# Optimization experiments

Measured on AMD Instinct MI355X. Metric: run time of the kernel, lower is better.

## Reference

```python
import jax, jax.numpy as jnp
import numpy as np

N = 1024      # number of residues/tokens
D = 768       # node feature dim (heads * d_head)
H = 12        # heads
DH = D // H   # d_head = 64
DP = 128      # pair feature dim
SCALE = 0.125 # 1/sqrt(d_head)
EPS = 1e-5

def _ln(x, w, b):
    m = jnp.mean(x, axis=-1, keepdims=True)
    v = jnp.var(x, axis=-1, keepdims=True)
    return (x - m) * jax.lax.rsqrt(v + EPS) * w + b

def setup_inputs() -> dict:
    key = jax.random.key(0)
    ks = jax.random.split(key, 8)
    s = 0.02
    return {
        "node_feats": jax.random.normal(ks[0], (N, D), dtype=jnp.float32),
        "pair_feats": jax.random.normal(ks[1], (N, N, DP), dtype=jnp.float32),
        "ln_node_w": jnp.ones((D,), jnp.float32), "ln_node_b": jnp.zeros((D,), jnp.float32),
        "pair_ln_w": jnp.ones((DP,), jnp.float32), "pair_ln_b": jnp.zeros((DP,), jnp.float32),
        "qkv_W": jax.random.normal(ks[2], (D, 3 * D), dtype=jnp.float32) * s,
        "qkv_b": jnp.zeros((3 * D,), jnp.float32),
        "q_ln_w": jnp.ones((D,), jnp.float32), "q_ln_b": jnp.zeros((D,), jnp.float32),
        "k_ln_w": jnp.ones((D,), jnp.float32), "k_ln_b": jnp.zeros((D,), jnp.float32),
        "g_W": jax.random.normal(ks[3], (D, D), dtype=jnp.float32) * s,
        "g_b": jnp.zeros((D,), jnp.float32),
        "bias_W": jax.random.normal(ks[4], (DP, H), dtype=jnp.float32) * s,
        "bias_b": jnp.zeros((H,), jnp.float32),
        "out_W": jax.random.normal(ks[5], (D, D), dtype=jnp.float32) * s,
        "out_b": jnp.zeros((D,), jnp.float32),
        "mask": jax.random.bernoulli(ks[6], 0.9, (N, N)),
    }

def reference(node_feats, pair_feats, ln_node_w, ln_node_b, pair_ln_w, pair_ln_b,
              qkv_W, qkv_b, q_ln_w, q_ln_b, k_ln_w, k_ln_b,
              g_W, g_b, bias_W, bias_b, out_W, out_b, mask):
    x = _ln(node_feats, ln_node_w, ln_node_b)                 # [N, D]
    p = _ln(pair_feats, pair_ln_w, pair_ln_b)                 # [N, N, DP]
    q, k, v = jnp.split(x @ qkv_W + qkv_b, 3, axis=-1)        # each [N, D]
    q = _ln(q, q_ln_w, q_ln_b)
    k = _ln(k, k_ln_w, k_ln_b)
    g = x @ g_W + g_b                                         # [N, D]
    bias = jnp.einsum('ijp,ph->hij', p, bias_W) + bias_b[:, None, None]  # [H, N, N]
    bias = bias + jnp.where(mask[None, :, :], 0.0, -10000.0)
    q = q.reshape(N, H, DH); k = k.reshape(N, H, DH); v = v.reshape(N, H, DH)
    logits = jnp.einsum('ihd,jhd->hij', q, k) * SCALE + bias  # [H, N, N]
    attn = jax.nn.softmax(logits, axis=-1)
    out = jnp.einsum('hij,jhd->ihd', attn, v).reshape(N, D)   # [N, D]
    out = jax.nn.sigmoid(g) * out
    return out @ out_W + out_b
```

## Files before the change

### kernel.cpp

```cpp
#include <hip/hip_runtime.h>
#include <math.h>

#define N_TOK 1024
#define D_DIM 768
#define H_N   12
#define DH    64
#define DP    128
#define SCALE 0.125f
#define EPS   1e-5f
#define NN    (N_TOK * N_TOK)

__global__ __launch_bounds__(128) void prep_kernel(
    const float* __restrict__ pair_ln_w, const float* __restrict__ pair_ln_b,
    const float* __restrict__ bias_W, const float* __restrict__ bias_b,
    float* __restrict__ W2, float* __restrict__ S2cb)
{
    __shared__ float Ws[DP * H_N];
    __shared__ float slw[DP], slb[DP];
    int t = threadIdx.x;
    slw[t] = pair_ln_w[t];
    slb[t] = pair_ln_b[t];
    for (int idx = t; idx < DP * H_N; idx += 128) Ws[idx] = bias_W[idx];
    __syncthreads();
    for (int idx = t; idx < DP * H_N; idx += 128) {
        int c = idx / H_N;
        W2[idx] = slw[c] * Ws[idx];
    }
    if (t < 24) {
        int h = t % H_N;
        bool isS = t < H_N;
        float s = 0.f;
        for (int c = 0; c < DP; ++c)
            s += (isS ? slw[c] : slb[c]) * Ws[c * H_N + h];
        S2cb[t] = isS ? s : (s + bias_b[h]);
    }
}

__global__ __launch_bounds__(256) void ln_kernel(
    const float* __restrict__ in, float* __restrict__ out,
    int istride, int ostride,
    const float* __restrict__ w, const float* __restrict__ b)
{
    int row = blockIdx.x;
    int tid = threadIdx.x;
    const float* ip = in + (size_t)row * istride;
    float v0 = ip[tid], v1 = ip[tid + 256], v2 = ip[tid + 512];
    float s = v0 + v1 + v2;
    float q = v0 * v0 + v1 * v1 + v2 * v2;
    __shared__ float red[8];
    #pragma unroll
    for (int o = 32; o > 0; o >>= 1) {
        s += __shfl_down(s, o);
        q += __shfl_down(q, o);
    }
    int lane = tid & 63, wv = tid >> 6;
    if (lane == 0) { red[wv] = s; red[4 + wv] = q; }
    __syncthreads();
    if (tid == 0) {
        float ss = red[0] + red[1] + red[2] + red[3];
        float qq = red[4] + red[5] + red[6] + red[7];
        float mean = ss * (1.f / 768.f);
        float var = qq * (1.f / 768.f) - mean * mean;
        red[0] = mean;
        red[1] = rsqrtf(var + EPS);
    }
    __syncthreads();
    float mean = red[0], rstd = red[1];
    float* op = out + (size_t)row * ostride;
    op[tid]       = (v0 - mean) * rstd * w[tid]       + b[tid];
    op[tid + 256] = (v1 - mean) * rstd * w[tid + 256] + b[tid + 256];
    op[tid + 512] = (v2 - mean) * rstd * w[tid + 512] + b[tid + 512];
}

__global__ __launch_bounds__(256) void sgemm(
    const float* __restrict__ A, int lda,
    const float* __restrict__ B0, int ldb0, const float* __restrict__ bias0,
    const float* __restrict__ B1, int ldb1, const float* __restrict__ bias1,
    int split, float* __restrict__ C, int ldc, int K)
{
    __shared__ float As[16 * 68];
    __shared__ float Bs[16 * 68];
    int tid = threadIdx.x;
    int tx = tid & 15, ty = tid >> 4;
    int m0 = blockIdx.y * 64, n0 = blockIdx.x * 64;
    const float* Bp; const float* bp; int ldb, bcol0;
    if (n0 < split) { Bp = B0; bp = bias0; ldb = ldb0; bcol0 = n0; }
    else            { Bp = B1; bp = bias1; ldb = ldb1; bcol0 = n0 - split; }

    float acc[4][4] = {};
    int ar = tid >> 2, ak = (tid & 3) * 4;
    int bk = tid >> 4, bc = (tid & 15) * 4;

    for (int kt = 0; kt < K; kt += 16) {
        float4 av = *(const float4*)&A[(size_t)(m0 + ar) * lda + kt + ak];
        float4 bv = *(const float4*)&Bp[(size_t)(kt + bk) * ldb + bcol0 + bc];
        As[(ak + 0) * 68 + ar] = av.x;
        As[(ak + 1) * 68 + ar] = av.y;
        As[(ak + 2) * 68 + ar] = av.z;
        As[(ak + 3) * 68 + ar] = av.w;
        *(float4*)&Bs[bk * 68 + bc] = bv;
        __syncthreads();
        #pragma unroll
        for (int kk = 0; kk < 16; ++kk) {
            float4 a = *(const float4*)&As[kk * 68 + ty * 4];
            float4 b = *(const float4*)&Bs[kk * 68 + tx * 4];
            acc[0][0] += a.x * b.x; acc[0][1] += a.x * b.y; acc[0][2] += a.x * b.z; acc[0][3] += a.x * b.w;
            acc[1][0] += a.y * b.x; acc[1][1] += a.y * b.y; acc[1][2] += a.y * b.z; acc[1][3] += a.y * b.w;
            acc[2][0] += a.z * b.x; acc[2][1] += a.z * b.y; acc[2][2] += a.z * b.z; acc[2][3] += a.z * b.w;
            acc[3][0] += a.w * b.x; acc[3][1] += a.w * b.y; acc[3][2] += a.w * b.z; acc[3][3] += a.w * b.w;
        }
        __syncthreads();
    }
    float4 bb = *(const float4*)&bp[bcol0 + tx * 4];
    #pragma unroll
    for (int u = 0; u < 4; ++u) {
        float4 o;
        o.x = acc[u][0] + bb.x; o.y = acc[u][1] + bb.y;
        o.z = acc[u][2] + bb.z; o.w = acc[u][3] + bb.w;
        *(float4*)&C[(size_t)(m0 + ty * 4 + u) * ldc + n0 + tx * 4] = o;
    }
}

__global__ __launch_bounds__(256) void bias_kernel(
    const float* __restrict__ pair, const int* __restrict__ mask,
    const float* __restrict__ W2, const float* __restrict__ S2cb,
    float* __restrict__ biasbuf)
{
    __shared__ float sW2[DP * H_N];
    __shared__ float sS[H_N], sC[H_N];
    int tid = threadIdx.x;
    for (int t = tid; t < DP * H_N; t += 256) sW2[t] = W2[t];
    if (tid < H_N) { sS[tid] = S2cb[tid]; sC[tid] = S2cb[H_N + tid]; }
    __syncthreads();

    int gid = blockIdx.x * 256 + tid;
    const float4* p4 = (const float4*)(pair + (size_t)gid * DP);
    float sum = 0.f, ssq = 0.f;
    float dot[H_N];
    #pragma unroll
    for (int h = 0; h < H_N; ++h) dot[h] = 0.f;

    #pragma unroll 4
    for (int c4 = 0; c4 < 32; ++c4) {
        float4 v = p4[c4];
        float e[4] = { v.x, v.y, v.z, v.w };
        #pragma unroll
        for (int k = 0; k < 4; ++k) {
            float x = e[k];
            sum += x; ssq += x * x;
            const float* wp = &sW2[(c4 * 4 + k) * H_N];
            #pragma unroll
            for (int h = 0; h < H_N; ++h) dot[h] += x * wp[h];
        }
    }
    float mean = sum * (1.f / 128.f);
    float var  = ssq * (1.f / 128.f) - mean * mean;
    float rstd = rsqrtf(var + EPS);
    float mz = (mask[gid] != 0) ? 0.f : -10000.f;
    #pragma unroll
    for (int h = 0; h < H_N; ++h)
        biasbuf[(size_t)h * NN + gid] = (dot[h] - mean * sS[h]) * rstd + sC[h] + mz;
}

__global__ __launch_bounds__(256) void attn_kernel(
    const float* __restrict__ xw, const float* __restrict__ biasbuf,
    float* __restrict__ attn_out)
{
    const int h  = blockIdx.y;
    const int i0 = blockIdx.x * 16;
    const int tid = threadIdx.x;
    const int tx = tid & 15, ty = tid >> 4;

    __shared__ float Qs[16 * 65];
    __shared__ float Ks[32 * 65];
    __shared__ float Vs[32 * 68];
    __shared__ float Ps[16 * 33];

    {
        int r = tid >> 4, c4 = (tid & 15) * 4;
        float4 v = *(const float4*)(xw + (size_t)(i0 + r) * 3072 + h * 64 + c4);
        float* d = &Qs[r * 65 + c4];
        d[0] = v.x * SCALE; d[1] = v.y * SCALE; d[2] = v.z * SCALE; d[3] = v.w * SCALE;
    }

    float m = -1e30f, l = 0.f;
    float a0 = 0.f, a1 = 0.f, a2 = 0.f, a3 = 0.f;
    const float* brow = biasbuf + (size_t)h * NN + (size_t)(i0 + ty) * N_TOK;

    for (int j0 = 0; j0 < N_TOK; j0 += 32) {
        #pragma unroll
        for (int q2 = 0; q2 < 2; ++q2) {
            int idx = tid + q2 * 256;
            int r = idx >> 4, c4 = (idx & 15) * 4;
            const float* kb = xw + (size_t)(j0 + r) * 3072 + 768 + h * 64 + c4;
            float4 kv = *(const float4*)kb;
            float* kd = &Ks[r * 65 + c4];
            kd[0] = kv.x; kd[1] = kv.y; kd[2] = kv.z; kd[3] = kv.w;
            float4 vv = *(const float4*)(kb + 768);
            *(float4*)&Vs[r * 68 + c4] = vv;
        }
        __syncthreads();

        float s0 = 0.f, s1 = 0.f;
        const float* qrow = &Qs[ty * 65];
        const float* k0 = &Ks[(2 * tx) * 65];
        const float* k1 = k0 + 65;
        #pragma unroll
        for (int d = 0; d < 64; ++d) {
            float qv = qrow[d];
            s0 += qv * k0[d];
            s1 += qv * k1[d];
        }
        s0 += brow[j0 + 2 * tx];
        s1 += brow[j0 + 2 * tx + 1];

        float mt = fmaxf(s0, s1);
        #pragma unroll
        for (int o = 1; o < 16; o <<= 1) mt = fmaxf(mt, __shfl_xor(mt, o));
        float mn = fmaxf(m, mt);
        float al = __expf(m - mn);
        float p0 = __expf(s0 - mn);
        float p1 = __expf(s1 - mn);
        float rs = p0 + p1;
        #pragma unroll
        for (int o = 1; o < 16; o <<= 1) rs += __shfl_xor(rs, o);
        l = l * al + rs;
        m = mn;
        a0 *= al; a1 *= al; a2 *= al; a3 *= al;
        Ps[ty * 33 + 2 * tx]     = p0;
        Ps[ty * 33 + 2 * tx + 1] = p1;
        __syncthreads();

        const float* prow = &Ps[ty * 33];
        #pragma unroll
        for (int j = 0; j < 32; ++j) {
            float pv = prow[j];
            float4 vv = *(const float4*)&Vs[j * 68 + tx * 4];
            a0 += pv * vv.x; a1 += pv * vv.y; a2 += pv * vv.z; a3 += pv * vv.w;
        }
        __syncthreads();
    }

    float inv = 1.f / l;
    int row = i0 + ty;
    float4 gv = *(const float4*)(xw + (size_t)row * 3072 + 2304 + h * 64 + tx * 4);
    float* op = attn_out + (size_t)row * 768 + h * 64 + tx * 4;
    op[0] = a0 * inv / (1.f + __expf(-gv.x));
    op[1] = a1 * inv / (1.f + __expf(-gv.y));
    op[2] = a2 * inv / (1.f + __expf(-gv.z));
    op[3] = a3 * inv / (1.f + __expf(-gv.w));
}

extern "C" void kernel_launch(void* const* d_in, const int* in_sizes, int n_in,
                              void* d_out, int out_size, void* d_ws, size_t ws_size,
                              hipStream_t stream)
{
    const float* node      = (const float*)d_in[0];
    const float* pair      = (const float*)d_in[1];
    const float* ln_node_w = (const float*)d_in[2];
    const float* ln_node_b = (const float*)d_in[3];
    const float* pair_ln_w = (const float*)d_in[4];
    const float* pair_ln_b = (const float*)d_in[5];
    const float* qkv_W     = (const float*)d_in[6];
    const float* qkv_b     = (const float*)d_in[7];
    const float* q_ln_w    = (const float*)d_in[8];
    const float* q_ln_b    = (const float*)d_in[9];
    const float* k_ln_w    = (const float*)d_in[10];
    const float* k_ln_b    = (const float*)d_in[11];
    const float* g_W       = (const float*)d_in[12];
    const float* g_b       = (const float*)d_in[13];
    const float* bias_W    = (const float*)d_in[14];
    const float* bias_b    = (const float*)d_in[15];
    const float* out_W     = (const float*)d_in[16];
    const float* out_b     = (const float*)d_in[17];
    const int*   mask      = (const int*)d_in[18];
    float* out = (float*)d_out;

    float* ws      = (float*)d_ws;
    float* x       = ws;
    float* xw      = x + 786432;
    float* W2      = xw + 3145728;
    float* S2cb    = W2 + 1536;
    float* biasbuf = S2cb + 32;
    float* attn_o  = biasbuf + 12582912;

    prep_kernel<<<1, 128, 0, stream>>>(pair_ln_w, pair_ln_b, bias_W, bias_b, W2, S2cb);
    ln_kernel<<<1024, 256, 0, stream>>>(node, x, 768, 768, ln_node_w, ln_node_b);
    sgemm<<<dim3(48, 16), 256, 0, stream>>>(x, 768,
                                            qkv_W, 2304, qkv_b,
                                            g_W, 768, g_b,
                                            2304, xw, 3072, 768);
    ln_kernel<<<1024, 256, 0, stream>>>(xw, xw, 3072, 3072, q_ln_w, q_ln_b);
    ln_kernel<<<1024, 256, 0, stream>>>(xw + 768, xw + 768, 3072, 3072, k_ln_w, k_ln_b);
    bias_kernel<<<4096, 256, 0, stream>>>(pair, mask, W2, S2cb, biasbuf);
    attn_kernel<<<dim3(64, 12), 256, 0, stream>>>(xw, biasbuf, attn_o);
    sgemm<<<dim3(12, 16), 256, 0, stream>>>(attn_o, 768,
                                            out_W, 768, out_b,
                                            out_W, 768, out_b,
                                            1 << 30, out, 768, 768);
}
```

Measured before the change: 1.092 ms.

## Widen sgemm tiles, vectorize bias weight reads, swizzle K tile in attention

The sgemm tile grows from 64x64 to 64x128 with 4x8 accumulators per thread, raising register reuse but halving the grid (384 and 96 blocks). The bias kernel reads the 12 per-channel weights as three float4 shared-memory loads instead of scalar loads. The attention kernel stores K in an XOR-swizzled, unpadded shared layout so the QK dot product can use float4 loads without bank conflicts, splits the accumulators, and loads the bias pair as a float2. The smaller GEMM grids may underfill the GPU, and the bias kernel is likely bound by memory bandwidth anyway.

```diff
diff --git a/kernel.cpp b/kernel.cpp
--- a/kernel.cpp
+++ b/kernel.cpp
@@ -78,46 +78,57 @@
     const float* __restrict__ B1, int ldb1, const float* __restrict__ bias1,
     int split, float* __restrict__ C, int ldc, int K)
 {
-    __shared__ float As[16 * 68];
-    __shared__ float Bs[16 * 68];
+    __shared__ __align__(16) float As[16 * 68];
+    __shared__ __align__(16) float Bs[16 * 132];
     int tid = threadIdx.x;
     int tx = tid & 15, ty = tid >> 4;
-    int m0 = blockIdx.y * 64, n0 = blockIdx.x * 64;
+    int m0 = blockIdx.y * 64, n0 = blockIdx.x * 128;
     const float* Bp; const float* bp; int ldb, bcol0;
     if (n0 < split) { Bp = B0; bp = bias0; ldb = ldb0; bcol0 = n0; }
     else            { Bp = B1; bp = bias1; ldb = ldb1; bcol0 = n0 - split; }
 
-    float acc[4][4] = {};
+    float acc[4][8] = {};
     int ar = tid >> 2, ak = (tid & 3) * 4;
-    int bk = tid >> 4, bc = (tid & 15) * 4;
+    int bk = tid >> 5, bc = (tid & 31) * 4;
 
     for (int kt = 0; kt < K; kt += 16) {
-        float4 av = *(const float4*)&A[(size_t)(m0 + ar) * lda + kt + ak];
-        float4 bv = *(const float4*)&Bp[(size_t)(kt + bk) * ldb + bcol0 + bc];
+        float4 av  = *(const float4*)&A[(size_t)(m0 + ar) * lda + kt + ak];
+        float4 b0v = *(const float4*)&Bp[(size_t)(kt + bk) * ldb + bcol0 + bc];
+        float4 b1v = *(const float4*)&Bp[(size_t)(kt + bk + 8) * ldb + bcol0 + bc];
         As[(ak + 0) * 68 + ar] = av.x;
         As[(ak + 1) * 68 + ar] = av.y;
         As[(ak + 2) * 68 + ar] = av.z;
         As[(ak + 3) * 68 + ar] = av.w;
-        *(float4*)&Bs[bk * 68 + bc] = bv;
+        *(float4*)&Bs[bk * 132 + bc] = b0v;
+        *(float4*)&Bs[(bk + 8) * 132 + bc] = b1v;
         __syncthreads();
         #pragma unroll
         for (int kk = 0; kk < 16; ++kk) {
-            float4 a = *(const float4*)&As[kk * 68 + ty * 4];
-            float4 b = *(const float4*)&Bs[kk * 68 + tx * 4];
-            acc[0][0] += a.x * b.x; acc[0][1] += a.x * b.y; acc[0][2] += a.x * b.z; acc[0][3] += a.x * b.w;
-            acc[1][0] += a.y * b.x; acc[1][1] += a.y * b.y; acc[1][2] += a.y * b.z; acc[1][3] += a.y * b.w;
-            acc[2][0] += a.z * b.x; acc[2][1] += a.z * b.y; acc[2][2] += a.z * b.z; acc[2][3] += a.z * b.w;
-            acc[3][0] += a.w * b.x; acc[3][1] += a.w * b.y; acc[3][2] += a.w * b.z; acc[3][3] += a.w * b.w;
-        }
-        __syncthreads();
-    }
-    float4 bb = *(const float4*)&bp[bcol0 + tx * 4];
+            float4 a  = *(const float4*)&As[kk * 68 + ty * 4];
+            float4 b0 = *(const float4*)&Bs[kk * 132 + tx * 4];
+            float4 b1 = *(const float4*)&Bs[kk * 132 + 64 + tx * 4];
+            float av_[4] = { a.x, a.y, a.z, a.w };
+            float bv_[8] = { b0.x, b0.y, b0.z, b0.w, b1.x, b1.y, b1.z, b1.w };
+            #pragma unroll
+            for (int u = 0; u < 4; ++u)
+                #pragma unroll
+                for (int i = 0; i < 8; ++i)
+                    acc[u][i] += av_[u] * bv_[i];
+        }
+        __syncthreads();
+    }
+    float4 bb0 = *(const float4*)&bp[bcol0 + tx * 4];
+    float4 bb1 = *(const float4*)&bp[bcol0 + 64 + tx * 4];
     #pragma unroll
     for (int u = 0; u < 4; ++u) {
-        float4 o;
-        o.x = acc[u][0] + bb.x; o.y = acc[u][1] + bb.y;
-        o.z = acc[u][2] + bb.z; o.w = acc[u][3] + bb.w;
-        *(float4*)&C[(size_t)(m0 + ty * 4 + u) * ldc + n0 + tx * 4] = o;
+        float* cp = &C[(size_t)(m0 + ty * 4 + u) * ldc + n0];
+        float4 o0, o1;
+        o0.x = acc[u][0] + bb0.x; o0.y = acc[u][1] + bb0.y;
+        o0.z = acc[u][2] + bb0.z; o0.w = acc[u][3] + bb0.w;
+        o1.x = acc[u][4] + bb1.x; o1.y = acc[u][5] + bb1.y;
+        o1.z = acc[u][6] + bb1.z; o1.w = acc[u][7] + bb1.w;
+        *(float4*)&cp[tx * 4]      = o0;
+        *(float4*)&cp[64 + tx * 4] = o1;
     }
 }
 
@@ -126,7 +137,7 @@
     const float* __restrict__ W2, const float* __restrict__ S2cb,
     float* __restrict__ biasbuf)
 {
-    __shared__ float sW2[DP * H_N];
+    __shared__ __align__(16) float sW2[DP * H_N];
     __shared__ float sS[H_N], sC[H_N];
     int tid = threadIdx.x;
     for (int t = tid; t < DP * H_N; t += 256) sW2[t] = W2[t];
@@ -148,9 +159,11 @@
         for (int k = 0; k < 4; ++k) {
             float x = e[k];
             sum += x; ssq += x * x;
-            const float* wp = &sW2[(c4 * 4 + k) * H_N];
-            #pragma unroll
-            for (int h = 0; h < H_N; ++h) dot[h] += x * wp[h];
+            const float4* wp4 = (const float4*)&sW2[(c4 * 4 + k) * H_N];
+            float4 w0 = wp4[0], w1 = wp4[1], w2 = wp4[2];
+            dot[0] += x * w0.x; dot[1] += x * w0.y; dot[2]  += x * w0.z; dot[3]  += x * w0.w;
+            dot[4] += x * w1.x; dot[5] += x * w1.y; dot[6]  += x * w1.z; dot[7]  += x * w1.w;
+            dot[8] += x * w2.x; dot[9] += x * w2.y; dot[10] += x * w2.z; dot[11] += x * w2.w;
         }
     }
     float mean = sum * (1.f / 128.f);
@@ -171,48 +184,54 @@
     const int tid = threadIdx.x;
     const int tx = tid & 15, ty = tid >> 4;
 
-    __shared__ float Qs[16 * 65];
-    __shared__ float Ks[32 * 65];
-    __shared__ float Vs[32 * 68];
+    __shared__ __align__(16) float Qs[16 * 68];
+    __shared__ __align__(16) float Ks[32 * 64];
+    __shared__ __align__(16) float Vs[32 * 68];
     __shared__ float Ps[16 * 33];
 
     {
-        int r = tid >> 4, c4 = (tid & 15) * 4;
-        float4 v = *(const float4*)(xw + (size_t)(i0 + r) * 3072 + h * 64 + c4);
-        float* d = &Qs[r * 65 + c4];
+        int r = tid >> 4, c4 = tid & 15;
+        float4 v = *(const float4*)(xw + (size_t)(i0 + r) * 3072 + h * 64 + c4 * 4);
+        float* d = &Qs[r * 68 + c4 * 4];
         d[0] = v.x * SCALE; d[1] = v.y * SCALE; d[2] = v.z * SCALE; d[3] = v.w * SCALE;
     }
 
     float m = -1e30f, l = 0.f;
     float a0 = 0.f, a1 = 0.f, a2 = 0.f, a3 = 0.f;
     const float* brow = biasbuf + (size_t)h * NN + (size_t)(i0 + ty) * N_TOK;
+    const int swz = tx & 7;
+    const float* qrow = &Qs[ty * 68];
+    const float* k0p = &Ks[(2 * tx) << 6];
+    const float* k1p = &Ks[((2 * tx) << 6) + 64];
 
     for (int j0 = 0; j0 < N_TOK; j0 += 32) {
         #pragma unroll
         for (int q2 = 0; q2 < 2; ++q2) {
             int idx = tid + q2 * 256;
-            int r = idx >> 4, c4 = (idx & 15) * 4;
-            const float* kb = xw + (size_t)(j0 + r) * 3072 + 768 + h * 64 + c4;
-            float4 kv = *(const float4*)kb;
-            float* kd = &Ks[r * 65 + c4];
-            kd[0] = kv.x; kd[1] = kv.y; kd[2] = kv.z; kd[3] = kv.w;
-            float4 vv = *(const float4*)(kb + 768);
-            *(float4*)&Vs[r * 68 + c4] = vv;
-        }
-        __syncthreads();
-
-        float s0 = 0.f, s1 = 0.f;
-        const float* qrow = &Qs[ty * 65];
-        const float* k0 = &Ks[(2 * tx) * 65];
-        const float* k1 = k0 + 65;
-        #pragma unroll
-        for (int d = 0; d < 64; ++d) {
-            float qv = qrow[d];
-            s0 += qv * k0[d];
-            s1 += qv * k1[d];
-        }
-        s0 += brow[j0 + 2 * tx];
-        s1 += brow[j0 + 2 * tx + 1];
+            int r = idx >> 4, c4 = idx & 15;
+            const float* gp = xw + (size_t)(j0 + r) * 3072 + 768 + h * 64 + c4 * 4;
+            float4 kv = *(const float4*)gp;
+            *(float4*)&Ks[(r << 6) + ((c4 ^ ((r >> 1) & 7)) << 2)] = kv;
+            float4 vv = *(const float4*)(gp + 768);
+            *(float4*)&Vs[r * 68 + c4 * 4] = vv;
+        }
+        __syncthreads();
+
+        float s0a = 0.f, s0b = 0.f, s1a = 0.f, s1b = 0.f;
+        #pragma unroll
+        for (int d4 = 0; d4 < 16; ++d4) {
+            float4 q  = *(const float4*)&qrow[d4 << 2];
+            int o = (d4 ^ swz) << 2;
+            float4 ka = *(const float4*)&k0p[o];
+            float4 kb = *(const float4*)&k1p[o];
+            s0a += q.x * ka.x + q.y * ka.y;
+            s0b += q.z * ka.z + q.w * ka.w;
+            s1a += q.x * kb.x + q.y * kb.y;
+            s1b += q.z * kb.z + q.w * kb.w;
+        }
+        float2 bb = *(const float2*)&brow[j0 + 2 * tx];
+        float s0 = s0a + s0b + bb.x;
+        float s1 = s1a + s1b + bb.y;
 
         float mt = fmaxf(s0, s1);
         #pragma unroll
@@ -286,7 +305,7 @@
 
     prep_kernel<<<1, 128, 0, stream>>>(pair_ln_w, pair_ln_b, bias_W, bias_b, W2, S2cb);
     ln_kernel<<<1024, 256, 0, stream>>>(node, x, 768, 768, ln_node_w, ln_node_b);
-    sgemm<<<dim3(48, 16), 256, 0, stream>>>(x, 768,
+    sgemm<<<dim3(24, 16), 256, 0, stream>>>(x, 768,
                                             qkv_W, 2304, qkv_b,
                                             g_W, 768, g_b,
                                             2304, xw, 3072, 768);
@@ -294,8 +313,8 @@
     ln_kernel<<<1024, 256, 0, stream>>>(xw + 768, xw + 768, 3072, 3072, k_ln_w, k_ln_b);
     bias_kernel<<<4096, 256, 0, stream>>>(pair, mask, W2, S2cb, biasbuf);
     attn_kernel<<<dim3(64, 12), 256, 0, stream>>>(xw, biasbuf, attn_o);
-    sgemm<<<dim3(12, 16), 256, 0, stream>>>(attn_o, 768,
-                                            out_W, 768, out_b,
-                                            out_W, 768, out_b,
-                                            1 << 30, out, 768, 768);
-}
+    sgemm<<<dim3(6, 16), 256, 0, stream>>>(attn_o, 768,
+                                           out_W, 768, out_b,
+                                           out_W, 768, out_b,
+                                           1 << 30, out, 768, 768);
+}
```

Measured after the change: 1.094 ms. About the same (+0.1%).
